# Performance work log

Measured on AMD Instinct MI355X. Metric: run time of the kernel, lower is better.

Reference implementation:

```python
import jax, jax.numpy as jnp
import numpy as np

HIDDEN = 4096
NUM_EXPERTS = 64
TOP_K = 2


def setup_inputs() -> dict:
    key = jax.random.key(0)
    k1, k2, k3 = jax.random.split(key, 3)
    hidden_states = jax.random.normal(k1, (4, 4096, HIDDEN), dtype=jnp.float32)
    # nn.Linear(hidden_size, num_experts): weight [num_experts, hidden], bias [num_experts]
    bound = 1.0 / np.sqrt(HIDDEN)
    gate_w = jax.random.uniform(k2, (NUM_EXPERTS, HIDDEN), dtype=jnp.float32, minval=-bound, maxval=bound)
    gate_b = jax.random.uniform(k3, (NUM_EXPERTS,), dtype=jnp.float32, minval=-bound, maxval=bound)
    return {"hidden_states": hidden_states, "gate_w": gate_w, "gate_b": gate_b}


def reference(hidden_states, gate_w, gate_b):
    b, s, h = hidden_states.shape
    x = hidden_states.reshape(-1, h)                      # [N, H], N = b*s
    router_logits = jnp.einsum('nh,eh->ne', x, gate_w) + gate_b  # [N, E]
    top_logits, selected_experts = jax.lax.top_k(router_logits, TOP_K)  # [N, K]
    routing_weights = jax.nn.softmax(top_logits, axis=-1)  # [N, K]
    aux_loss = jnp.float32(0.0)
    return routing_weights, selected_experts, router_logits, aux_loss
```

## Files before the change

### kernel.cpp

```cpp
#include <hip/hip_runtime.h>
#include <math.h>
#include <stdint.h>

#define HIDDEN  4096
#define NEXP    64
#define TOKS    64
#define KCH     128
#define NCHK    (HIDDEN / KCH)
#define XREG_FL (TOKS * KCH)
#define PAR_FL  16384

typedef __bf16 bf16x8 __attribute__((ext_vector_type(8)));
typedef float  f32x4  __attribute__((ext_vector_type(4)));

union BfU { uint4 u; bf16x8 b; };

static __device__ __forceinline__ void cvt_hilo(const float* x8, bf16x8& hi, bf16x8& lo) {
#pragma unroll
    for (int j = 0; j < 8; ++j) {
        const float x = x8[j];
        const __bf16 h = (__bf16)x;
        const float  r = x - (float)h;
        hi[j] = h;
        lo[j] = (__bf16)r;
    }
}

__device__ __forceinline__ void gload_lds16(const void* g, void* l) {
    __builtin_amdgcn_global_load_lds(
        (const __attribute__((address_space(1))) void*)g,
        (__attribute__((address_space(3))) void*)l, 16, 0, 0);
}

__global__ __launch_bounds__(512) void wconv_kernel(
    const float* __restrict__ W, ushort* __restrict__ wsHi, ushort* __restrict__ wsLo)
{
    const int gid = blockIdx.x * 512 + threadIdx.x;
    const int S = gid >> 8;
    const int e = (gid >> 6) & 3;
    const int l = gid & 63;
    const int row = 16 * e + (l & 15);
    const int k0  = 32 * S + 8 * (l >> 4);
    const float* src = W + (size_t)row * HIDDEN + k0;
    float x8[8];
    *(float4*)&x8[0] = *(const float4*)src;
    *(float4*)&x8[4] = *(const float4*)(src + 4);
    BfU hi, lo;
    cvt_hilo(x8, hi.b, lo.b);
    const size_t o = ((size_t)(S * 4 + e) * 64 + l) * 8;
    *(uint4*)(wsHi + o) = hi.u;
    *(uint4*)(wsLo + o) = lo.u;
}

__global__ __launch_bounds__(1024, 1) void router_mfma_kernel(
    const float* __restrict__ X,
    const ushort* __restrict__ wsHi, const ushort* __restrict__ wsLo,
    const float* __restrict__ Bv, float* __restrict__ out, int nTok)
{
    __shared__ float smem[2 * PAR_FL];

    const int tid = threadIdx.x;
    const int wv  = tid >> 6;
    const int tg  = wv >> 2;
    const int kh  = wv & 3;
    const int l   = tid & 63;
    const int g   = l >> 4;
    const int cr  = l & 15;
    const int t0  = blockIdx.x * TOKS;

    const float* XgS[2];
    int xdst[2];
#pragma unroll
    for (int r = 0; r < 2; ++r) {
        const int q   = 2 * wv + r;
        const int row = 2 * q + (l >> 5);
        XgS[r]  = X + (size_t)(t0 + row) * HIDDEN + (((l & 31) ^ (row & 7)) << 2);
        xdst[r] = 2 * q * KCH;
    }
    const ushort* BhS = wsHi + (size_t)wv * 512 + (size_t)l * 8;
    const ushort* BlS = wsLo + (size_t)wv * 512 + (size_t)l * 8;
    const int bhdst = XREG_FL + wv * 256;
    const int bldst = XREG_FL + 4096 + wv * 256;

    const int m8   = cr & 7;
    const int rowX = (16 * tg + cr) * KCH;
    const int gA0  = (8 * kh + ((2 * g + 0) ^ m8)) << 2;
    const int gA1  = (8 * kh + ((2 * g + 1) ^ m8)) << 2;

    f32x4 acc[4] = {{0.f,0.f,0.f,0.f},{0.f,0.f,0.f,0.f},{0.f,0.f,0.f,0.f},{0.f,0.f,0.f,0.f}};

#pragma unroll
    for (int r = 0; r < 2; ++r) gload_lds16(XgS[r], smem + xdst[r]);
    gload_lds16(BhS, smem + bhdst);
    gload_lds16(BlS, smem + bldst);

#pragma unroll 1
    for (int c = 0; c < NCHK; ++c) {
        asm volatile("s_waitcnt vmcnt(0)" ::: "memory");
        __syncthreads();
        const int p = c & 1;
        if (c + 1 < NCHK) {
            float* pb = smem + ((c + 1) & 1) * PAR_FL;
            const int ko = (c + 1) * KCH;
            const size_t bo = (size_t)(c + 1) * 8192;
#pragma unroll
            for (int r = 0; r < 2; ++r) gload_lds16(XgS[r] + ko, pb + xdst[r]);
            gload_lds16(BhS + bo, pb + bhdst);
            gload_lds16(BlS + bo, pb + bldst);
        }
        const float*  xb = smem + p * PAR_FL + rowX;
        const ushort* bh = (const ushort*)(smem + p * PAR_FL + XREG_FL) + (4 * kh) * 512 + l * 8;
        const ushort* bl = bh + 8192;
        float x8[8];
        *(float4*)&x8[0] = *(const float4*)(xb + gA0);
        *(float4*)&x8[4] = *(const float4*)(xb + gA1);
        bf16x8 xh, xo; cvt_hilo(x8, xh, xo);
#pragma unroll
        for (int e = 0; e < 4; ++e) {
            BfU ph, pl;
            ph.u = *(const uint4*)(bh + e * 512);
            pl.u = *(const uint4*)(bl + e * 512);
            acc[e] = __builtin_amdgcn_mfma_f32_16x16x32_bf16(xh, ph.b, acc[e], 0, 0, 0);
            acc[e] = __builtin_amdgcn_mfma_f32_16x16x32_bf16(xo, ph.b, acc[e], 0, 0, 0);
            acc[e] = __builtin_amdgcn_mfma_f32_16x16x32_bf16(xh, pl.b, acc[e], 0, 0, 0);
        }
    }

    __syncthreads();

    float (*tiles)[64][68] = (float (*)[64][68])smem;
    float* tt = smem + 4 * 64 * 68;

#pragma unroll
    for (int e = 0; e < 4; ++e)
#pragma unroll
        for (int i = 0; i < 4; ++i)
            tiles[kh][16 * tg + 4 * g + i][16 * e + cr] = acc[e][i];
    __syncthreads();

    const size_t offSel = (size_t)nTok * 2;
    const size_t offLog = (size_t)nTok * 4;

    {
        const int tok = tid >> 4;
        const int e4  = (tid & 15) * 4;
        const float4 s0 = *(const float4*)&tiles[0][tok][e4];
        const float4 s1 = *(const float4*)&tiles[1][tok][e4];
        const float4 s2 = *(const float4*)&tiles[2][tok][e4];
        const float4 s3 = *(const float4*)&tiles[3][tok][e4];
        const float4 bb = *(const float4*)(Bv + e4);
        const float4 r = make_float4(s0.x + s1.x + s2.x + s3.x + bb.x,
                                     s0.y + s1.y + s2.y + s3.y + bb.y,
                                     s0.z + s1.z + s2.z + s3.z + bb.z,
                                     s0.w + s1.w + s2.w + s3.w + bb.w);
        *(float4*)(out + offLog + (size_t)(t0 + tok) * NEXP + e4) = r;
        tt[(e4 + 0) * 65 + tok] = r.x;
        tt[(e4 + 1) * 65 + tok] = r.y;
        tt[(e4 + 2) * 65 + tok] = r.z;
        tt[(e4 + 3) * 65 + tok] = r.w;
    }
    __syncthreads();

    if (tid < 64) {
        const int t = tid;
        float m1 = -INFINITY, m2 = -INFINITY;
        int i1 = 0, i2 = 0;
#pragma unroll
        for (int e = 0; e < NEXP; ++e) {
            const float v = tt[e * 65 + t];
            if (v > m1)      { m2 = m1; i2 = i1; m1 = v; i1 = e; }
            else if (v > m2) { m2 = v; i2 = e; }
        }
        const float ex  = expf(m2 - m1);
        const float inv = 1.0f / (1.0f + ex);
        *(float2*)(out + (size_t)(t0 + t) * 2)          = make_float2(inv, ex * inv);
        *(float2*)(out + offSel + (size_t)(t0 + t) * 2) = make_float2((float)i1, (float)i2);
    }

    if (blockIdx.x == 0 && tid == 0)
        out[offLog + (size_t)nTok * NEXP] = 0.0f;
}

extern "C" void kernel_launch(void* const* d_in, const int* in_sizes, int n_in,
                              void* d_out, int out_size, void* d_ws, size_t ws_size,
                              hipStream_t stream)
{
    const float* X  = (const float*)d_in[0];
    const float* W  = (const float*)d_in[1];
    const float* Bv = (const float*)d_in[2];
    float* out = (float*)d_out;
    const int nTok = in_sizes[0] / HIDDEN;
    ushort* wsHi = (ushort*)d_ws;
    ushort* wsLo = wsHi + (size_t)NEXP * HIDDEN;

    wconv_kernel<<<64, 512, 0, stream>>>(W, wsHi, wsLo);
    router_mfma_kernel<<<nTok / TOKS, 1024, 0, stream>>>(X, wsHi, wsLo, Bv, out, nTok);
}
```

Measured before the change: 70.78 us.

## Shrink router blocks to 32 tokens, 512 threads, two blocks per CU

Halves the token tile and the K chunk so each block uses 512 threads and less LDS, with launch bounds asking for two resident blocks per CU. Warps are split into a 2x2 grid over experts and K halves instead of four K splits, so the cross-warp reduction sums two partial tiles instead of four. The weight conversion kernel now launches 256 blocks of 128 threads. The goal is more blocks in flight (512 instead of 256) for better CU coverage and latency hiding. The cost is twice as many K-loop iterations and barriers, and the converted weights are re-fetched by twice as many blocks.

```diff
diff --git a/kernel.cpp b/kernel.cpp
--- a/kernel.cpp
+++ b/kernel.cpp
@@ -2,13 +2,13 @@
 #include <math.h>
 #include <stdint.h>
 
-#define HIDDEN  4096
-#define NEXP    64
-#define TOKS    64
-#define KCH     128
-#define NCHK    (HIDDEN / KCH)
-#define XREG_FL (TOKS * KCH)
-#define PAR_FL  16384
+#define HIDDEN 4096
+#define NEXP   64
+#define TOKS   32
+#define KCH    64
+#define NCHK   (HIDDEN / KCH)
+#define X_FL   (TOKS * KCH)
+#define PAR_FL (X_FL + 2 * 2048)
 
 typedef __bf16 bf16x8 __attribute__((ext_vector_type(8)));
 typedef float  f32x4  __attribute__((ext_vector_type(4)));
@@ -35,7 +35,7 @@
 __global__ __launch_bounds__(512) void wconv_kernel(
     const float* __restrict__ W, ushort* __restrict__ wsHi, ushort* __restrict__ wsLo)
 {
-    const int gid = blockIdx.x * 512 + threadIdx.x;
+    const int gid = blockIdx.x * blockDim.x + threadIdx.x;
     const int S = gid >> 8;
     const int e = (gid >> 6) & 3;
     const int l = gid & 63;
@@ -52,7 +52,7 @@
     *(uint4*)(wsLo + o) = lo.u;
 }
 
-__global__ __launch_bounds__(1024, 1) void router_mfma_kernel(
+__global__ __launch_bounds__(512, 2) void router_mfma_kernel(
     const float* __restrict__ X,
     const ushort* __restrict__ wsHi, const ushort* __restrict__ wsLo,
     const float* __restrict__ Bv, float* __restrict__ out, int nTok)
@@ -62,35 +62,30 @@
     const int tid = threadIdx.x;
     const int wv  = tid >> 6;
     const int tg  = wv >> 2;
-    const int kh  = wv & 3;
+    const int eh  = (wv >> 1) & 1;
+    const int kh  = wv & 1;
     const int l   = tid & 63;
     const int g   = l >> 4;
     const int cr  = l & 15;
     const int t0  = blockIdx.x * TOKS;
 
-    const float* XgS[2];
-    int xdst[2];
-#pragma unroll
-    for (int r = 0; r < 2; ++r) {
-        const int q   = 2 * wv + r;
-        const int row = 2 * q + (l >> 5);
-        XgS[r]  = X + (size_t)(t0 + row) * HIDDEN + (((l & 31) ^ (row & 7)) << 2);
-        xdst[r] = 2 * q * KCH;
-    }
+    const int srow = 4 * wv + (l >> 4);
+    const int sgr  = (l & 8) | ((l & 7) ^ (srow & 7));
+    const float* XgS = X + (size_t)(t0 + srow) * HIDDEN + sgr * 4;
+    const int xdst  = wv * 256;
     const ushort* BhS = wsHi + (size_t)wv * 512 + (size_t)l * 8;
     const ushort* BlS = wsLo + (size_t)wv * 512 + (size_t)l * 8;
-    const int bhdst = XREG_FL + wv * 256;
-    const int bldst = XREG_FL + 4096 + wv * 256;
+    const int bhdst = X_FL + wv * 256;
+    const int bldst = X_FL + 2048 + wv * 256;
 
     const int m8   = cr & 7;
     const int rowX = (16 * tg + cr) * KCH;
-    const int gA0  = (8 * kh + ((2 * g + 0) ^ m8)) << 2;
-    const int gA1  = (8 * kh + ((2 * g + 1) ^ m8)) << 2;
+    const int rdA0 = rowX + 4 * (8 * kh + ((2 * g + 0) ^ m8));
+    const int rdA1 = rowX + 4 * (8 * kh + ((2 * g + 1) ^ m8));
 
-    f32x4 acc[4] = {{0.f,0.f,0.f,0.f},{0.f,0.f,0.f,0.f},{0.f,0.f,0.f,0.f},{0.f,0.f,0.f,0.f}};
+    f32x4 acc[2] = {{0.f,0.f,0.f,0.f},{0.f,0.f,0.f,0.f}};
 
-#pragma unroll
-    for (int r = 0; r < 2; ++r) gload_lds16(XgS[r], smem + xdst[r]);
+    gload_lds16(XgS, smem + xdst);
     gload_lds16(BhS, smem + bhdst);
     gload_lds16(BlS, smem + bldst);
 
@@ -101,25 +96,23 @@
         const int p = c & 1;
         if (c + 1 < NCHK) {
             float* pb = smem + ((c + 1) & 1) * PAR_FL;
-            const int ko = (c + 1) * KCH;
-            const size_t bo = (size_t)(c + 1) * 8192;
-#pragma unroll
-            for (int r = 0; r < 2; ++r) gload_lds16(XgS[r] + ko, pb + xdst[r]);
-            gload_lds16(BhS + bo, pb + bhdst);
-            gload_lds16(BlS + bo, pb + bldst);
+            gload_lds16(XgS + (c + 1) * KCH, pb + xdst);
+            gload_lds16(BhS + (size_t)(c + 1) * 4096, pb + bhdst);
+            gload_lds16(BlS + (size_t)(c + 1) * 4096, pb + bldst);
         }
-        const float*  xb = smem + p * PAR_FL + rowX;
-        const ushort* bh = (const ushort*)(smem + p * PAR_FL + XREG_FL) + (4 * kh) * 512 + l * 8;
-        const ushort* bl = bh + 8192;
+        const float*  xb = smem + p * PAR_FL;
+        const ushort* bh = (const ushort*)(smem + p * PAR_FL + X_FL) + kh * 2048 + l * 8;
+        const ushort* bl = bh + 4096;
         float x8[8];
-        *(float4*)&x8[0] = *(const float4*)(xb + gA0);
-        *(float4*)&x8[4] = *(const float4*)(xb + gA1);
+        *(float4*)&x8[0] = *(const float4*)(xb + rdA0);
+        *(float4*)&x8[4] = *(const float4*)(xb + rdA1);
         bf16x8 xh, xo; cvt_hilo(x8, xh, xo);
 #pragma unroll
-        for (int e = 0; e < 4; ++e) {
+        for (int e = 0; e < 2; ++e) {
+            const int e2 = 2 * eh + e;
             BfU ph, pl;
-            ph.u = *(const uint4*)(bh + e * 512);
-            pl.u = *(const uint4*)(bl + e * 512);
+            ph.u = *(const uint4*)(bh + e2 * 512);
+            pl.u = *(const uint4*)(bl + e2 * 512);
             acc[e] = __builtin_amdgcn_mfma_f32_16x16x32_bf16(xh, ph.b, acc[e], 0, 0, 0);
             acc[e] = __builtin_amdgcn_mfma_f32_16x16x32_bf16(xo, ph.b, acc[e], 0, 0, 0);
             acc[e] = __builtin_amdgcn_mfma_f32_16x16x32_bf16(xh, pl.b, acc[e], 0, 0, 0);
@@ -128,14 +121,16 @@
 
     __syncthreads();
 
-    float (*tiles)[64][68] = (float (*)[64][68])smem;
-    float* tt = smem + 4 * 64 * 68;
+    float (*tiles)[32][68] = (float (*)[32][68])smem;
+    float* tt = smem + 4608;
 
 #pragma unroll
-    for (int e = 0; e < 4; ++e)
+    for (int e = 0; e < 2; ++e) {
+        const int e2 = 2 * eh + e;
 #pragma unroll
         for (int i = 0; i < 4; ++i)
-            tiles[kh][16 * tg + 4 * g + i][16 * e + cr] = acc[e][i];
+            tiles[kh][16 * tg + 4 * g + i][16 * e2 + cr] = acc[e][i];
+    }
     __syncthreads();
 
     const size_t offSel = (size_t)nTok * 2;
@@ -146,28 +141,24 @@
         const int e4  = (tid & 15) * 4;
         const float4 s0 = *(const float4*)&tiles[0][tok][e4];
         const float4 s1 = *(const float4*)&tiles[1][tok][e4];
-        const float4 s2 = *(const float4*)&tiles[2][tok][e4];
-        const float4 s3 = *(const float4*)&tiles[3][tok][e4];
         const float4 bb = *(const float4*)(Bv + e4);
-        const float4 r = make_float4(s0.x + s1.x + s2.x + s3.x + bb.x,
-                                     s0.y + s1.y + s2.y + s3.y + bb.y,
-                                     s0.z + s1.z + s2.z + s3.z + bb.z,
-                                     s0.w + s1.w + s2.w + s3.w + bb.w);
+        const float4 r = make_float4(s0.x + s1.x + bb.x, s0.y + s1.y + bb.y,
+                                     s0.z + s1.z + bb.z, s0.w + s1.w + bb.w);
         *(float4*)(out + offLog + (size_t)(t0 + tok) * NEXP + e4) = r;
-        tt[(e4 + 0) * 65 + tok] = r.x;
-        tt[(e4 + 1) * 65 + tok] = r.y;
-        tt[(e4 + 2) * 65 + tok] = r.z;
-        tt[(e4 + 3) * 65 + tok] = r.w;
+        tt[(e4 + 0) * 33 + tok] = r.x;
+        tt[(e4 + 1) * 33 + tok] = r.y;
+        tt[(e4 + 2) * 33 + tok] = r.z;
+        tt[(e4 + 3) * 33 + tok] = r.w;
     }
     __syncthreads();
 
-    if (tid < 64) {
+    if (tid < TOKS) {
         const int t = tid;
         float m1 = -INFINITY, m2 = -INFINITY;
         int i1 = 0, i2 = 0;
 #pragma unroll
         for (int e = 0; e < NEXP; ++e) {
-            const float v = tt[e * 65 + t];
+            const float v = tt[e * 33 + t];
             if (v > m1)      { m2 = m1; i2 = i1; m1 = v; i1 = e; }
             else if (v > m2) { m2 = v; i2 = e; }
         }
@@ -193,6 +184,6 @@
     ushort* wsHi = (ushort*)d_ws;
     ushort* wsLo = wsHi + (size_t)NEXP * HIDDEN;
 
-    wconv_kernel<<<64, 512, 0, stream>>>(W, wsHi, wsLo);
-    router_mfma_kernel<<<nTok / TOKS, 1024, 0, stream>>>(X, wsHi, wsLo, Bv, out, nTok);
+    wconv_kernel<<<256, 128, 0, stream>>>(W, wsHi, wsLo);
+    router_mfma_kernel<<<nTok / TOKS, 512, 0, stream>>>(X, wsHi, wsLo, Bv, out, nTok);
 }
```

After: 84.70 us. 1.2x slower.

## Prefetch two chunks ahead with partial vmcnt waits in router GEMM

Applied to the files above, without the earlier changes.

The main loop now issues loads for chunks 0 and 1 up front and, each iteration, waits only for the older chunk (vmcnt(4)) before computing. The refill for chunk c+2 is issued after a second barrier, once the current buffer has been consumed. This keeps two loads in flight instead of one, hiding more global latency. The wconv launch also changes from 64x512 to 256x128 blocks, with blockDim used for indexing. The risk is a second barrier per iteration and raw s_barrier without a full waitcnt on LDS.

```diff
diff --git a/kernel.cpp b/kernel.cpp
--- a/kernel.cpp
+++ b/kernel.cpp
@@ -7,7 +7,7 @@
 #define TOKS    64
 #define KCH     128
 #define NCHK    (HIDDEN / KCH)
-#define XREG_FL (TOKS * KCH)
+#define X_FL    (TOKS * KCH)
 #define PAR_FL  16384
 
 typedef __bf16 bf16x8 __attribute__((ext_vector_type(8)));
@@ -35,7 +35,7 @@
 __global__ __launch_bounds__(512) void wconv_kernel(
     const float* __restrict__ W, ushort* __restrict__ wsHi, ushort* __restrict__ wsLo)
 {
-    const int gid = blockIdx.x * 512 + threadIdx.x;
+    const int gid = blockIdx.x * blockDim.x + threadIdx.x;
     const int S = gid >> 8;
     const int e = (gid >> 6) & 3;
     const int l = gid & 63;
@@ -79,8 +79,8 @@
     }
     const ushort* BhS = wsHi + (size_t)wv * 512 + (size_t)l * 8;
     const ushort* BlS = wsLo + (size_t)wv * 512 + (size_t)l * 8;
-    const int bhdst = XREG_FL + wv * 256;
-    const int bldst = XREG_FL + 4096 + wv * 256;
+    const int bhdst = X_FL + wv * 256;
+    const int bldst = X_FL + 4096 + wv * 256;
 
     const int m8   = cr & 7;
     const int rowX = (16 * tg + cr) * KCH;
@@ -93,36 +93,44 @@
     for (int r = 0; r < 2; ++r) gload_lds16(XgS[r], smem + xdst[r]);
     gload_lds16(BhS, smem + bhdst);
     gload_lds16(BlS, smem + bldst);
+#pragma unroll
+    for (int r = 0; r < 2; ++r) gload_lds16(XgS[r] + KCH, smem + PAR_FL + xdst[r]);
+    gload_lds16(BhS + 8192, smem + PAR_FL + bhdst);
+    gload_lds16(BlS + 8192, smem + PAR_FL + bldst);
 
 #pragma unroll 1
     for (int c = 0; c < NCHK; ++c) {
-        asm volatile("s_waitcnt vmcnt(0)" ::: "memory");
-        __syncthreads();
+        if (c + 1 < NCHK) asm volatile("s_waitcnt vmcnt(4)" ::: "memory");
+        else              asm volatile("s_waitcnt vmcnt(0)" ::: "memory");
+        __builtin_amdgcn_s_barrier();
         const int p = c & 1;
-        if (c + 1 < NCHK) {
-            float* pb = smem + ((c + 1) & 1) * PAR_FL;
-            const int ko = (c + 1) * KCH;
-            const size_t bo = (size_t)(c + 1) * 8192;
+        {
+            const float*  xb = smem + p * PAR_FL;
+            const ushort* bh = (const ushort*)(xb + X_FL) + (4 * kh) * 512 + l * 8;
+            const ushort* bl = bh + 8192;
+            float x8[8];
+            *(float4*)&x8[0] = *(const float4*)(xb + rowX + gA0);
+            *(float4*)&x8[4] = *(const float4*)(xb + rowX + gA1);
+            bf16x8 xh, xo; cvt_hilo(x8, xh, xo);
+#pragma unroll
+            for (int e = 0; e < 4; ++e) {
+                BfU ph, pl;
+                ph.u = *(const uint4*)(bh + e * 512);
+                pl.u = *(const uint4*)(bl + e * 512);
+                acc[e] = __builtin_amdgcn_mfma_f32_16x16x32_bf16(xh, ph.b, acc[e], 0, 0, 0);
+                acc[e] = __builtin_amdgcn_mfma_f32_16x16x32_bf16(xo, ph.b, acc[e], 0, 0, 0);
+                acc[e] = __builtin_amdgcn_mfma_f32_16x16x32_bf16(xh, pl.b, acc[e], 0, 0, 0);
+            }
+        }
+        __builtin_amdgcn_s_barrier();
+        if (c + 2 < NCHK) {
+            float* pb = smem + p * PAR_FL;
+            const int ko = (c + 2) * KCH;
+            const size_t bo = (size_t)(c + 2) * 8192;
 #pragma unroll
             for (int r = 0; r < 2; ++r) gload_lds16(XgS[r] + ko, pb + xdst[r]);
             gload_lds16(BhS + bo, pb + bhdst);
             gload_lds16(BlS + bo, pb + bldst);
-        }
-        const float*  xb = smem + p * PAR_FL + rowX;
-        const ushort* bh = (const ushort*)(smem + p * PAR_FL + XREG_FL) + (4 * kh) * 512 + l * 8;
-        const ushort* bl = bh + 8192;
-        float x8[8];
-        *(float4*)&x8[0] = *(const float4*)(xb + gA0);
-        *(float4*)&x8[4] = *(const float4*)(xb + gA1);
-        bf16x8 xh, xo; cvt_hilo(x8, xh, xo);
-#pragma unroll
-        for (int e = 0; e < 4; ++e) {
-            BfU ph, pl;
-            ph.u = *(const uint4*)(bh + e * 512);
-            pl.u = *(const uint4*)(bl + e * 512);
-            acc[e] = __builtin_amdgcn_mfma_f32_16x16x32_bf16(xh, ph.b, acc[e], 0, 0, 0);
-            acc[e] = __builtin_amdgcn_mfma_f32_16x16x32_bf16(xo, ph.b, acc[e], 0, 0, 0);
-            acc[e] = __builtin_amdgcn_mfma_f32_16x16x32_bf16(xh, pl.b, acc[e], 0, 0, 0);
         }
     }
 
@@ -193,6 +201,6 @@
     ushort* wsHi = (ushort*)d_ws;
     ushort* wsLo = wsHi + (size_t)NEXP * HIDDEN;
 
-    wconv_kernel<<<64, 512, 0, stream>>>(W, wsHi, wsLo);
+    wconv_kernel<<<256, 128, 0, stream>>>(W, wsHi, wsLo);
     router_mfma_kernel<<<nTok / TOKS, 1024, 0, stream>>>(X, wsHi, wsLo, Bv, out, nTok);
 }
```

New measurement: 70.63 us. About the same (-0.2%).
